# Kernel optimization log

Measured on AMD Instinct MI355X. Metric: run time of the kernel, lower is better.

Reference implementation:

```python
import jax, jax.numpy as jnp
import numpy as np

B, S, DM, H = 2, 2048, 1024, 16
HD = DM // H
SCALE = 1.0 / np.sqrt(HD)  # temperature = 1.0
LN_EPS = 1e-5


def setup_inputs() -> dict:
    key = jax.random.key(0)
    ks = jax.random.split(key, 12)
    s = 1.0 / np.sqrt(DM)
    inp = {
        'x': jax.random.normal(ks[0], (B, S, DM), dtype=jnp.float32),
        'Wq': jax.random.uniform(ks[1], (DM, DM), jnp.float32, -s, s),
        'bq': jnp.zeros((DM,), jnp.float32),
        'Wk': jax.random.uniform(ks[2], (DM, DM), jnp.float32, -s, s),
        'bk': jnp.zeros((DM,), jnp.float32),
        'Wv': jax.random.uniform(ks[3], (DM, DM), jnp.float32, -s, s),
        'bv': jnp.zeros((DM,), jnp.float32),
        'Wo': jax.random.uniform(ks[4], (DM, DM), jnp.float32, -s, s),
        'bo': jnp.zeros((DM,), jnp.float32),
        'Wg': jax.random.uniform(ks[5], (DM, DM), jnp.float32, -s, s),
        'bg': jnp.zeros((DM,), jnp.float32),
        'attention_weights': jnp.ones((H,), jnp.float32),
        'ln_gamma': jnp.ones((DM,), jnp.float32),
        'ln_beta': jnp.zeros((DM,), jnp.float32),
    }
    return inp


def _forward(x, Wq, bq, Wk, bk, Wv, bv, Wo, bo, Wg, bg, attention_weights, ln_gamma, ln_beta):
    # projections -> [B, H, S, HD]
    def split_heads(t):
        return t.reshape(B, S, H, HD).transpose(0, 2, 1, 3)
    q = split_heads(x @ Wq.T + bq)
    k = split_heads(x @ Wk.T + bk)
    v = split_heads(x @ Wv.T + bv)
    # scores [B, H, S, S]; no softmax: exact-erf GELU activation instead
    scores = jnp.einsum('bhsd,bhtd->bhst', q, k) * SCALE
    attn = jax.nn.gelu(scores, approximate=False)
    head_w = jax.nn.softmax(attention_weights)  # [H]
    attn = attn * head_w[None, :, None, None]
    # context [B, S, DM]
    ctx = jnp.einsum('bhst,bhtd->bhsd', attn, v).transpose(0, 2, 1, 3).reshape(B, S, DM)
    out = ctx @ Wo.T + bo
    gate = jax.nn.sigmoid(out @ Wg.T + bg)
    out = gate * out + (1.0 - gate) * x
    y = out + x
    mu = jnp.mean(y, axis=-1, keepdims=True)
    var = jnp.var(y, axis=-1, keepdims=True)
    return (y - mu) / jnp.sqrt(var + LN_EPS) * ln_gamma + ln_beta


def reference(x, Wq, bq, Wk, bk, Wv, bv, Wo, bo, Wg, bg, attention_weights, ln_gamma, ln_beta):
    return _forward(x, Wq, bq, Wk, bk, Wv, bv, Wo, bo, Wg, bg, attention_weights, ln_gamma, ln_beta)
```

## Files before the change

kernel.cpp:

```cpp
#include <hip/hip_runtime.h>
#include <hip/hip_bf16.h>

#define B_ 2
#define S_ 2048
#define DM_ 1024
#define H_ 16
#define HD_ 64
#define QKVLD 3072
#define WELT_ ((size_t)DM_ * DM_)

using bf16x8 = __attribute__((ext_vector_type(8))) short;
using f16x2  = __attribute__((ext_vector_type(2))) _Float16;
using f16x8  = __attribute__((ext_vector_type(8))) _Float16;
using f32x4  = __attribute__((ext_vector_type(4))) float;
using f32x16 = __attribute__((ext_vector_type(16))) float;

#define GLOAD16(g, l) __builtin_amdgcn_global_load_lds( \
    (const __attribute__((address_space(1))) void*)(g), \
    (__attribute__((address_space(3))) void*)(l), 16, 0, 0)

__device__ __forceinline__ int swz128(int row, int bytecol) {
    return row * 128 + (bytecol ^ ((row & 7) << 4));
}

__device__ __forceinline__ ushort bf16_rne(float f) {
    uint b = __builtin_bit_cast(uint, f);
    b += 0x7FFF + ((b >> 16) & 1);
    return (ushort)(b >> 16);
}

__device__ __forceinline__ float bf16_to_f(ushort u) {
    return __builtin_bit_cast(float, (uint)u << 16);
}

__device__ __forceinline__ void pl32swap(uint& a, uint& b) {
    asm volatile("v_permlane32_swap_b32 %0, %1" : "+v"(a), "+v"(b));
}

__device__ __forceinline__ f16x2 cvt_pk_f16(float lo, float hi) {
    return __builtin_bit_cast(f16x2, __builtin_amdgcn_cvt_pkrtz(lo, hi));
}

__device__ __forceinline__ f16x2 gelu_h2(f16x2 x) {
    const f16x2 C3 = {(_Float16)-0.00074855f, (_Float16)-0.00074855f};
    const f16x2 C2 = {(_Float16)0.0146724f,   (_Float16)0.0146724f};
    const f16x2 C1 = {(_Float16)-0.1266945f,  (_Float16)-0.1266945f};
    const f16x2 C0 = {(_Float16)0.7966101f,   (_Float16)0.7966101f};
    const f16x2 ONE = {(_Float16)1.0f, (_Float16)1.0f};
    const f16x2 NEG = {(_Float16)-1.0f, (_Float16)-1.0f};
    const f16x2 HLF = {(_Float16)0.5f, (_Float16)0.5f};
    f16x2 u = x * x;
    f16x2 t = C3 * u + C2;
    t = t * u + C1;
    t = t * u + C0;
    f16x2 e = x * t;
    e = __builtin_elementwise_min(__builtin_elementwise_max(e, NEG), ONE);
    f16x2 hx = x * HLF;
    return hx * e + hx;
}

__global__ __launch_bounds__(256) void prep_kernel(
    const float* __restrict__ x, __hip_bfloat16* __restrict__ xb,
    const float* __restrict__ Wq, const float* __restrict__ Wk, const float* __restrict__ Wv,
    const float* __restrict__ Wo, const float* __restrict__ Wg,
    const float* __restrict__ bq, const float* __restrict__ bk, const float* __restrict__ bv,
    const float* __restrict__ bo, const float* __restrict__ bg,
    const float* __restrict__ aw, __hip_bfloat16* __restrict__ Wall,
    __hip_bfloat16* __restrict__ Wcomb, __hip_bfloat16* __restrict__ Wot,
    float* __restrict__ bqkv, float* __restrict__ bcomb)
{
    __shared__ ushort stile[64][72];
    auto headw = [&](int h) {
        float mx = aw[0];
        for (int i = 1; i < H_; ++i) mx = fmaxf(mx, aw[i]);
        float sm = 0.f;
        for (int i = 0; i < H_; ++i) sm += expf(aw[i] - mx);
        return expf(aw[h] - mx) / sm;
    };
    const int tid = threadIdx.x;
    int blk = blockIdx.x;
    if (blk < 4096) {
        int i = blk * 1024 + tid * 4;
        float4 v = *(const float4*)(x + i);
        ushort4 o = { bf16_rne(v.x), bf16_rne(v.y), bf16_rne(v.z), bf16_rne(v.w) };
        *(ushort4*)(xb + i) = o;
    } else if (blk < 9216) {
        blk -= 4096;
        int widx = blk >> 10;
        int row = blk & 1023;
        int off = row * 1024 + tid * 4;
        const float* src = widx == 0 ? Wq : widx == 1 ? Wk : widx == 2 ? Wv : widx == 3 ? Wo : Wg;
        float scale = widx == 0 ? 0.125f : 1.0f;
        if (widx == 2) scale = headw(row >> 6);
        __hip_bfloat16* dst = (widx == 3) ? Wcomb
                            : Wall + (size_t)(widx == 4 ? 3 : widx) * WELT_;
        float4 v = *(const float4*)(src + off);
        ushort4 o = { bf16_rne(v.x * scale), bf16_rne(v.y * scale),
                      bf16_rne(v.z * scale), bf16_rne(v.w * scale) };
        *(ushort4*)(dst + off) = o;
    } else if (blk < 9228) {
        int i = (blk - 9216) * 256 + tid;
        if (i < 3 * DM_) {
            float v;
            if (i < DM_) v = bq[i] * 0.125f;
            else if (i < 2 * DM_) v = bk[i - DM_];
            else v = bv[i - 2 * DM_] * headw((i - 2 * DM_) >> 6);
            bqkv[i] = v;
        }
    } else if (blk < 9484) {
        int idx = blk - 9228;
        const int c0 = (idx & 15) * 64, r0 = (idx >> 4) * 64;
#pragma unroll
        for (int c = tid; c < 1024; c += 256) {
            int row = c >> 4, cg = c & 15;
            float4 v = *(const float4*)(Wo + (size_t)(r0 + row) * 1024 + c0 + cg * 4);
            stile[row][cg * 4 + 0] = bf16_rne(v.x);
            stile[row][cg * 4 + 1] = bf16_rne(v.y);
            stile[row][cg * 4 + 2] = bf16_rne(v.z);
            stile[row][cg * 4 + 3] = bf16_rne(v.w);
        }
        __syncthreads();
#pragma unroll
        for (int c = tid; c < 512; c += 256) {
            int d = c >> 3, tg = c & 7;
            union { ushort u[8]; float4 v; } tmp;
#pragma unroll
            for (int j = 0; j < 8; ++j) tmp.u[j] = stile[tg * 8 + j][d];
            *(float4*)(Wot + (size_t)(c0 + d) * 1024 + r0 + tg * 8) = tmp.v;
        }
    } else {
        int idx = blk - 9484;
        const int w = tid >> 6, lane = tid & 63;
        if (idx < 4) bcomb[idx * 256 + tid] = bo[idx * 256 + tid];
        const int row = idx * 4 + w;
        float s = 0.f;
        for (int k = lane; k < 1024; k += 64) s += Wg[row * 1024 + k] * bo[k];
#pragma unroll
        for (int off = 32; off > 0; off >>= 1) s += __shfl_down(s, off, 64);
        if (lane == 0) bcomb[1024 + row] = bg[row] + s;
    }
}

__global__ __launch_bounds__(256, 2) void gemm_nt_kernel(
    const __hip_bfloat16* __restrict__ A, int lda,
    const __hip_bfloat16* __restrict__ Bw, int ldb,
    const float* __restrict__ bias, float* __restrict__ Cf,
    __hip_bfloat16* __restrict__ Cb, int ldc, int K, int gx1, int nblk1,
    const __hip_bfloat16* __restrict__ A2, const __hip_bfloat16* __restrict__ B2,
    __hip_bfloat16* __restrict__ C2)
{
    __shared__ __align__(16) char smem[32768];
    const int tid = threadIdx.x;
    const int w = tid >> 6, lane = tid & 63, hi = lane >> 4, lo = lane & 15;
    const int wr = w >> 1, wc = w & 1;

    const int bid = blockIdx.x;
    const __hip_bfloat16 *Ap, *Bp;
    const float* bp;
    float* cf;
    __hip_bfloat16* cb;
    int LDA, LDB, LDC, KK, bx, by;
    if (bid < nblk1) {
        bx = bid % gx1; by = bid / gx1;
        Ap = A; Bp = Bw; bp = bias; cf = Cf; cb = Cb;
        LDA = lda; LDB = ldb; LDC = ldc; KK = K;
    } else {
        int t2 = bid - nblk1;
        bx = t2 & 7; by = t2 >> 3;
        Ap = A2; Bp = B2; bp = nullptr; cf = nullptr; cb = C2;
        LDA = DM_; LDB = DM_; LDC = DM_; KK = DM_;
    }
    const int m0 = by * 128, n0 = bx * 128;

    const int srow = lane >> 3;
    const int scol = (lane & 7) ^ srow;
    const __hip_bfloat16* sbase;
    int sld;
    char* lbase;
    if (w < 2) {
        sbase = Ap + (size_t)(m0 + w * 64 + srow) * LDA + scol * 8;
        sld = LDA;
        lbase = smem + w * 8192;
    } else {
        sbase = Bp + (size_t)(n0 + (w - 2) * 64 + srow) * LDB + scol * 8;
        sld = LDB;
        lbase = smem + 16384 + (w - 2) * 8192;
    }

    f32x4 acc[4][4];
#pragma unroll
    for (int m = 0; m < 4; ++m)
#pragma unroll
        for (int n = 0; n < 4; ++n) acc[m][n] = (f32x4){0.f, 0.f, 0.f, 0.f};

    for (int k0 = 0; k0 < KK; k0 += 64) {
#pragma unroll
        for (int i = 0; i < 8; ++i)
            GLOAD16(sbase + (size_t)i * 8 * sld + k0, lbase + i * 1024);
        __syncthreads();
#pragma unroll
        for (int ks = 0; ks < 2; ++ks) {
            bf16x8 af[4], bfr[4];
#pragma unroll
            for (int m = 0; m < 4; ++m)
                af[m] = *(const bf16x8*)(smem + swz128(wr * 64 + m * 16 + lo, ks * 64 + hi * 16));
#pragma unroll
            for (int n = 0; n < 4; ++n)
                bfr[n] = *(const bf16x8*)(smem + 16384 + swz128(wc * 64 + n * 16 + lo, ks * 64 + hi * 16));
#pragma unroll
            for (int m = 0; m < 4; ++m)
#pragma unroll
                for (int n = 0; n < 4; ++n)
                    acc[m][n] = __builtin_amdgcn_mfma_f32_16x16x32_bf16(af[m], bfr[n], acc[m][n], 0, 0, 0);
        }
        __syncthreads();
    }

#pragma unroll
    for (int n = 0; n < 4; ++n) {
        int gc = n0 + wc * 64 + n * 16 + lo;
        float bz = bp ? bp[gc] : 0.f;
#pragma unroll
        for (int m = 0; m < 4; ++m) {
            int gr = m0 + wr * 64 + m * 16 + hi * 4;
#pragma unroll
            for (int r = 0; r < 4; ++r) {
                float v = acc[m][n][r] + bz;
                size_t o = (size_t)(gr + r) * LDC + gc;
                if (cf) cf[o] = v;
                if (cb) *(ushort*)(cb + o) = bf16_rne(v);
            }
        }
    }
}

__global__ __launch_bounds__(256) void transpose_v_kernel(const __hip_bfloat16* __restrict__ QKV,
                                                          _Float16* __restrict__ Vt) {
    __shared__ __align__(16) ushort tile[64][80];
    const int tid = threadIdx.x;
    const int nt = S_ / 64;
    const int blk = blockIdx.x;
    const int t0 = (blk % nt) * 64;
    const int bh = blk / nt;
    const int h = bh % H_, b = bh / H_;
#pragma unroll
    for (int c = tid; c < 512; c += 256) {
        int row = c >> 3, cg = c & 7;
        float4 v = *(const float4*)(QKV + (size_t)(b * S_ + t0 + row) * QKVLD + 2 * DM_ + h * HD_ + cg * 8);
        *(float4*)(&tile[row][cg * 8]) = v;
    }
    __syncthreads();
#pragma unroll
    for (int c = tid; c < 512; c += 256) {
        int d = c >> 3, tg = c & 7;
        union { _Float16 h16[8]; float4 v; } tmp;
#pragma unroll
        for (int j = 0; j < 8; ++j)
            tmp.h16[j] = (_Float16)bf16_to_f(tile[tg * 8 + j][d]);
        *(float4*)(Vt + ((size_t)(b * H_ + h) * HD_ + d) * S_ + t0 + tg * 8) = tmp.v;
    }
}

__global__ __launch_bounds__(512) void attn_kernel(
    const __hip_bfloat16* __restrict__ QKV, const _Float16* __restrict__ Vt,
    __hip_bfloat16* __restrict__ ctx)
{
    __shared__ __align__(16) char lds[2][32768];

    const int tid = threadIdx.x;
    const int w = tid >> 6, lane = tid & 63;
    const int l31 = lane & 31, hi2 = lane >> 5;
    const int qg = w & 3, th = w >> 2;
    const int nq = S_ / 128;
    int blk = blockIdx.x;
    blk = (blk & 7) * 64 + (blk >> 3);
    const int q0 = (blk % nq) * 128;
    const int bh = blk / nq;
    const int h = bh % H_, b = bh / H_;

    bf16x8 qf[4];
    {
        const __hip_bfloat16* qrow = QKV + ((size_t)(b * S_ + q0 + qg * 32 + l31) * QKVLD + h * HD_);
#pragma unroll
        for (int ks = 0; ks < 4; ++ks)
            qf[ks] = *(const bf16x8*)(qrow + ks * 16 + hi2 * 8);
    }

    const bool isK = (w < 4);
    const int f0 = (isK ? w : (w - 4)) * 4;
    const char* sp[4];
    int loff[4];
#pragma unroll
    for (int j = 0; j < 4; ++j) {
        int f = f0 + j;
        if (isK) {
            sp[j] = (const char*)(QKV + (size_t)(b * S_ + (f >> 2) * 32 + l31) * QKVLD + DM_ + h * HD_ + (f & 3) * 16 + hi2 * 8);
            loff[j] = f * 1024;
        } else {
            sp[j] = (const char*)(Vt + ((size_t)((b * H_ + h) * HD_) + (f >> 3) * 32 + l31) * S_ + (f & 7) * 16 + hi2 * 8);
            loff[j] = 16384 + f * 1024;
        }
    }
    const size_t tstep = isK ? (size_t)256 * QKVLD : (size_t)256;

#define STAGE(buf) do { \
    _Pragma("unroll") \
    for (int j = 0; j < 4; ++j) { \
        GLOAD16(sp[j], lds[buf] + loff[j]); \
        sp[j] += tstep; \
    } } while (0)

    f32x16 cacc[2];
#pragma unroll
    for (int n = 0; n < 2; ++n)
#pragma unroll
        for (int r = 0; r < 16; ++r) cacc[n][r] = 0.f;

    STAGE(0);
    asm volatile("s_waitcnt vmcnt(0)" ::: "memory");
    __builtin_amdgcn_s_barrier();

    const int lane16 = lane * 16;
    const int NT = S_ / 128;
    for (int t = 0; t < NT; ++t) {
        const int cur = t & 1;
        if (t + 1 < NT) STAGE(cur ^ 1);

        __builtin_amdgcn_s_setprio(1);
#pragma unroll
        for (int tci = 0; tci < 2; ++tci) {
            const int tc = th * 2 + tci;
            f32x16 sacc;
#pragma unroll
            for (int r = 0; r < 16; ++r) sacc[r] = 0.f;
#pragma unroll
            for (int ks = 0; ks < 4; ++ks) {
                bf16x8 kf = *(const bf16x8*)(lds[cur] + (tc * 4 + ks) * 1024 + lane16);
                sacc = __builtin_amdgcn_mfma_f32_32x32x16_bf16(kf, qf[ks], sacc, 0, 0, 0);
            }
            f16x2 P[8];
#pragma unroll
            for (int i = 0; i < 8; ++i)
                P[i] = gelu_h2(cvt_pk_f16(sacc[2 * i], sacc[2 * i + 1]));
            uint a0 = __builtin_bit_cast(uint, P[0]), b0 = __builtin_bit_cast(uint, P[2]);
            uint a1 = __builtin_bit_cast(uint, P[1]), b1 = __builtin_bit_cast(uint, P[3]);
            uint a2 = __builtin_bit_cast(uint, P[4]), b2 = __builtin_bit_cast(uint, P[6]);
            uint a3 = __builtin_bit_cast(uint, P[5]), b3 = __builtin_bit_cast(uint, P[7]);
            pl32swap(a0, b0); pl32swap(a1, b1); pl32swap(a2, b2); pl32swap(a3, b3);
            union { uint u[4]; f16x8 v; } pa0, pa1;
            pa0.u[0] = a0; pa0.u[1] = a1; pa0.u[2] = b0; pa0.u[3] = b1;
            pa1.u[0] = a2; pa1.u[1] = a3; pa1.u[2] = b2; pa1.u[3] = b3;
#pragma unroll
            for (int kc2 = 0; kc2 < 2; ++kc2) {
                int kc = tc * 2 + kc2;
                f16x8 pa = kc2 ? pa1.v : pa0.v;
#pragma unroll
                for (int n2 = 0; n2 < 2; ++n2) {
                    f16x8 vf = *(const f16x8*)(lds[cur] + 16384 + (n2 * 8 + kc) * 1024 + lane16);
                    cacc[n2] = __builtin_amdgcn_mfma_f32_32x32x16_f16(pa, vf, cacc[n2], 0, 0, 0);
                }
            }
        }
        __builtin_amdgcn_s_setprio(0);
        asm volatile("s_waitcnt vmcnt(0)" ::: "memory");
        __builtin_amdgcn_s_barrier();
    }

    char* red = lds[0];
    if (th == 1) {
#pragma unroll
        for (int n2 = 0; n2 < 2; ++n2)
#pragma unroll
            for (int r = 0; r < 16; ++r)
                *(float*)(red + qg * 8192 + (n2 * 16 + r) * 256 + lane * 4) = cacc[n2][r];
    }
    __syncthreads();
    if (th == 0) {
#pragma unroll
        for (int n2 = 0; n2 < 2; ++n2)
#pragma unroll
            for (int r = 0; r < 16; ++r) {
                float v = cacc[n2][r] +
                    *(const float*)(red + qg * 8192 + (n2 * 16 + r) * 256 + lane * 4);
                int qrow = (r & 3) + 8 * (r >> 2) + 4 * hi2;
                size_t o = (size_t)(b * S_ + q0 + qg * 32 + qrow) * DM_ + h * HD_ + n2 * 32 + l31;
                *(ushort*)(ctx + o) = bf16_rne(v);
            }
    }
#undef STAGE
}

__global__ __launch_bounds__(256) void epilogue_ln_kernel(
    const __hip_bfloat16* __restrict__ og, const __hip_bfloat16* __restrict__ xb,
    const float* __restrict__ gamma, const float* __restrict__ beta,
    float* __restrict__ y)
{
    const int row = blockIdx.x, tid = threadIdx.x;
    const size_t obase = (size_t)row * 2048 + tid * 4;
    const size_t xbase = (size_t)row * DM_ + tid * 4;
    ushort4 ob = *(const ushort4*)(og + obase);
    ushort4 gb = *(const ushort4*)(og + obase + 1024);
    ushort4 xv = *(const ushort4*)(xb + xbase);
    float yv[4];
    float s = 0.f, s2 = 0.f;
    const ushort* obp = (const ushort*)&ob;
    const ushort* gbp = (const ushort*)&gb;
    const ushort* xp  = (const ushort*)&xv;
#pragma unroll
    for (int j = 0; j < 4; ++j) {
        float o = bf16_to_f(obp[j]), g = bf16_to_f(gbp[j]), xx = bf16_to_f(xp[j]);
        float gate = __builtin_amdgcn_rcpf(1.f + __expf(-g));
        float yy = gate * o + (1.f - gate) * xx + xx;
        yv[j] = yy;
        s += yy; s2 += yy * yy;
    }
    const int w = tid >> 6, lane = tid & 63;
#pragma unroll
    for (int off = 32; off > 0; off >>= 1) {
        s  += __shfl_down(s, off, 64);
        s2 += __shfl_down(s2, off, 64);
    }
    __shared__ float red[8];
    if (lane == 0) { red[w] = s; red[4 + w] = s2; }
    __syncthreads();
    s  = red[0] + red[1] + red[2] + red[3];
    s2 = red[4] + red[5] + red[6] + red[7];
    const float mu = s * (1.f / DM_);
    const float var = s2 * (1.f / DM_) - mu * mu;
    const float rstd = rsqrtf(var + 1e-5f);
    float4 outv;
#pragma unroll
    for (int j = 0; j < 4; ++j) {
        int col = tid * 4 + j;
        ((float*)&outv)[j] = (yv[j] - mu) * rstd * gamma[col] + beta[col];
    }
    *(float4*)(y + xbase) = outv;
}

extern "C" void kernel_launch(void* const* d_in, const int* in_sizes, int n_in,
                              void* d_out, int out_size, void* d_ws, size_t ws_size,
                              hipStream_t stream) {
    const float* x  = (const float*)d_in[0];
    const float* Wq = (const float*)d_in[1];
    const float* bq = (const float*)d_in[2];
    const float* Wk = (const float*)d_in[3];
    const float* bk = (const float*)d_in[4];
    const float* Wv = (const float*)d_in[5];
    const float* bv = (const float*)d_in[6];
    const float* Wo = (const float*)d_in[7];
    const float* bo = (const float*)d_in[8];
    const float* Wg = (const float*)d_in[9];
    const float* bg = (const float*)d_in[10];
    const float* aw = (const float*)d_in[11];
    const float* gamma = (const float*)d_in[12];
    const float* beta  = (const float*)d_in[13];

    char* ws = (char*)d_ws;
    size_t off = 0;
    auto alloc = [&](size_t bytes) -> char* {
        char* p = ws + off;
        off += (bytes + 255) & ~(size_t)255;
        return p;
    };
    const size_t NTOK = (size_t)B_ * S_;
    const size_t NELT = NTOK * DM_;

    __hip_bfloat16* xb    = (__hip_bfloat16*)alloc(NELT * 2);
    __hip_bfloat16* Wall  = (__hip_bfloat16*)alloc(4 * WELT_ * 2);
    __hip_bfloat16* Wot   = (__hip_bfloat16*)alloc(WELT_ * 2);
    __hip_bfloat16* Wcomb = (__hip_bfloat16*)alloc(2 * WELT_ * 2);
    float*          bqkv  = (float*)alloc(3 * DM_ * 4);
    float*          bcomb = (float*)alloc(2 * DM_ * 4);
    __hip_bfloat16* qkvb  = (__hip_bfloat16*)alloc(NTOK * QKVLD * 2);
    _Float16*       Vtb   = (_Float16*)alloc(NELT * 2);
    __hip_bfloat16* ctxb  = (__hip_bfloat16*)alloc(NELT * 2);
    __hip_bfloat16* ogb   = (__hip_bfloat16*)alloc(NTOK * 2048 * 2);

    prep_kernel<<<9740, 256, 0, stream>>>(x, xb, Wq, Wk, Wv, Wo, Wg,
                                          bq, bk, bv, bo, bg, aw,
                                          Wall, Wcomb, Wot, bqkv, bcomb);

    gemm_nt_kernel<<<768 + 64, 256, 0, stream>>>(
        xb, DM_, Wall, DM_, bqkv, nullptr, qkvb, QKVLD, DM_, 24, 768,
        Wall + 3 * WELT_, Wot, Wcomb + WELT_);

    transpose_v_kernel<<<B_ * H_ * (S_ / 64), 256, 0, stream>>>(qkvb, Vtb);
    attn_kernel<<<B_ * H_ * (S_ / 128), 512, 0, stream>>>(qkvb, Vtb, ctxb);

    gemm_nt_kernel<<<512, 256, 0, stream>>>(
        ctxb, DM_, Wcomb, DM_, bcomb, nullptr, ogb, 2048, DM_, 16, 1 << 30,
        nullptr, nullptr, nullptr);

    epilogue_ln_kernel<<<(int)NTOK, 256, 0, stream>>>(ogb, xb, gamma, beta, (float*)d_out);
}
```

Measured before the change: 140.2 us.

## Load K fragments directly from global into registers, keep only V in LDS

The attention kernel no longer stages K tiles through LDS. Each wave loads its own K fragments directly from global memory into registers every iteration, and only V is staged via global_load_lds double buffering, which halves the LDS footprint. This cuts LDS traffic and capacity pressure, possibly allowing higher occupancy. In exchange, K loads are no longer prefetched a tile ahead and are duplicated across the four query-group waves, so global/L2 load latency is exposed inside the loop.

```diff
diff --git a/kernel.cpp b/kernel.cpp
--- a/kernel.cpp
+++ b/kernel.cpp
@@ -265,7 +265,7 @@
     const __hip_bfloat16* __restrict__ QKV, const _Float16* __restrict__ Vt,
     __hip_bfloat16* __restrict__ ctx)
 {
-    __shared__ __align__(16) char lds[2][32768];
+    __shared__ __align__(16) char lds[2][16384];
 
     const int tid = threadIdx.x;
     const int w = tid >> 6, lane = tid & 63;
@@ -286,28 +286,25 @@
             qf[ks] = *(const bf16x8*)(qrow + ks * 16 + hi2 * 8);
     }
 
-    const bool isK = (w < 4);
-    const int f0 = (isK ? w : (w - 4)) * 4;
-    const char* sp[4];
-    int loff[4];
-#pragma unroll
-    for (int j = 0; j < 4; ++j) {
-        int f = f0 + j;
-        if (isK) {
-            sp[j] = (const char*)(QKV + (size_t)(b * S_ + (f >> 2) * 32 + l31) * QKVLD + DM_ + h * HD_ + (f & 3) * 16 + hi2 * 8);
-            loff[j] = f * 1024;
-        } else {
-            sp[j] = (const char*)(Vt + ((size_t)((b * H_ + h) * HD_) + (f >> 3) * 32 + l31) * S_ + (f & 7) * 16 + hi2 * 8);
-            loff[j] = 16384 + f * 1024;
-        }
-    }
-    const size_t tstep = isK ? (size_t)256 * QKVLD : (size_t)256;
+    const char* kp0 = (const char*)(QKV
+        + (size_t)(b * S_ + (th * 2 + 0) * 32 + l31) * QKVLD + DM_ + h * HD_ + hi2 * 8);
+    const char* kp1 = kp0 + (size_t)32 * QKVLD * 2;
+
+    const char* sp[2];
+    int loff[2];
+#pragma unroll
+    for (int j = 0; j < 2; ++j) {
+        int f = w * 2 + j;
+        sp[j] = (const char*)(Vt + ((size_t)((b * H_ + h) * HD_) + (f >> 3) * 32 + l31) * S_
+                              + (f & 7) * 16 + hi2 * 8);
+        loff[j] = f * 1024;
+    }
 
 #define STAGE(buf) do { \
     _Pragma("unroll") \
-    for (int j = 0; j < 4; ++j) { \
+    for (int j = 0; j < 2; ++j) { \
         GLOAD16(sp[j], lds[buf] + loff[j]); \
-        sp[j] += tstep; \
+        sp[j] += 256; \
     } } while (0)
 
     f32x16 cacc[2];
@@ -326,6 +323,15 @@
         const int cur = t & 1;
         if (t + 1 < NT) STAGE(cur ^ 1);
 
+        bf16x8 kfa[4], kfb[4];
+#pragma unroll
+        for (int ks = 0; ks < 4; ++ks) {
+            kfa[ks] = *(const bf16x8*)(kp0 + ks * 32);
+            kfb[ks] = *(const bf16x8*)(kp1 + ks * 32);
+        }
+        kp0 += (size_t)128 * QKVLD * 2;
+        kp1 += (size_t)128 * QKVLD * 2;
+
         __builtin_amdgcn_s_setprio(1);
 #pragma unroll
         for (int tci = 0; tci < 2; ++tci) {
@@ -335,7 +341,7 @@
             for (int r = 0; r < 16; ++r) sacc[r] = 0.f;
 #pragma unroll
             for (int ks = 0; ks < 4; ++ks) {
-                bf16x8 kf = *(const bf16x8*)(lds[cur] + (tc * 4 + ks) * 1024 + lane16);
+                bf16x8 kf = tci ? kfb[ks] : kfa[ks];
                 sacc = __builtin_amdgcn_mfma_f32_32x32x16_bf16(kf, qf[ks], sacc, 0, 0, 0);
             }
             f16x2 P[8];
@@ -356,7 +362,7 @@
                 f16x8 pa = kc2 ? pa1.v : pa0.v;
 #pragma unroll
                 for (int n2 = 0; n2 < 2; ++n2) {
-                    f16x8 vf = *(const f16x8*)(lds[cur] + 16384 + (n2 * 8 + kc) * 1024 + lane16);
+                    f16x8 vf = *(const f16x8*)(lds[cur] + (n2 * 8 + kc) * 1024 + lane16);
                     cacc[n2] = __builtin_amdgcn_mfma_f32_32x32x16_f16(pa, vf, cacc[n2], 0, 0, 0);
                 }
             }
@@ -366,7 +372,7 @@
         __builtin_amdgcn_s_barrier();
     }
 
-    char* red = lds[0];
+    char* red = (char*)lds;
     if (th == 1) {
 #pragma unroll
         for (int n2 = 0; n2 < 2; ++n2)
```

Measured after the change: 178.3 us. 1.27x slower.
